# Kernel optimization log

Hardware: AMD Instinct MI355X
Metric: run time of the kernel (lower is better)

## Reference

```python
import jax, jax.numpy as jnp
import numpy as np

BUFFER_SIZE = 1024
N_BANDS = 2049
N_SPEC = 4
FRAME_SIZE = 2 * (N_BANDS - 1)  # 4096
EPS = 1e-10


def _hann_periodic(n):
    k = np.arange(n, dtype=np.float64)
    return (0.5 * (1.0 - np.cos(2.0 * np.pi * k / n))).astype(np.float32)


def _build_windows():
    # Mirrors _build_windows with nonlinearity=0 (single filterbank).
    base = _hann_periodic(FRAME_SIZE) / (FRAME_SIZE / 4.0)
    win_scale = float(base.sum())
    wins = [base.copy()]
    for lvl in range(1, N_SPEC):
        stride = 1 << lvl
        small = base[::stride][: FRAME_SIZE // stride]
        w = np.zeros(FRAME_SIZE, dtype=np.float32)
        w[-(FRAME_SIZE // stride):] = small
        w *= win_scale / w.sum()
        wins.append(w)
    return [jnp.asarray(w) for w in wins]


WINDOWS = _build_windows()


def _forward(x):
    # x: (B, BUFFER_SIZE). Fresh (reset) state: time buffers are zeros,
    # spectrogram/left-boundary buffers are +1e6 (identity for min).
    B = x.shape[0]
    T = 1 << (N_SPEC - 1)  # finest time grid = output columns
    out = jnp.full((B, N_BANDS, T), 1.0e6, dtype=x.dtype)
    pad = jnp.zeros((B, FRAME_SIZE), dtype=x.dtype)
    concat = jnp.concatenate([pad, x], axis=-1)  # (B, FRAME_SIZE + BUFFER_SIZE)
    for lvl in range(N_SPEC):
        chunk = BUFFER_SIZE >> lvl
        nfr = 1 << lvl  # sub-frames at this level
        # Overlap-save sliding windows: frame i starts at offset chunk + i*chunk
        frames = jnp.stack(
            [concat[:, chunk + i * chunk: chunk + i * chunk + FRAME_SIZE] for i in range(nfr)],
            axis=1,
        )  # (B, nfr, FRAME_SIZE)
        spec = jnp.fft.rfft(frames * WINDOWS[lvl][None, None, :], n=FRAME_SIZE, axis=-1)
        power = jnp.transpose(spec.real ** 2 + spec.imag ** 2, (0, 2, 1))  # (B, N_BANDS, nfr)
        # Upsample coarse-time levels to the finest grid (tile replication, the
        # streaming moving-max/min buffers realize this in the original) and
        # take the min across scales (buffers initialised to 1e6 = +inf for min).
        out = jnp.minimum(out, jnp.repeat(power, T // nfr, axis=-1))
    return 10.0 * jnp.log10(jnp.maximum(out, EPS))  # power -> dB


def setup_inputs() -> dict:
    key = jax.random.key(0)
    x = jax.random.normal(key, (1024, BUFFER_SIZE), dtype=jnp.float32)
    return {"x": x}


def reference(x):
    return _forward(x)
```

## Files before the change

### kernel.cpp

```cpp
#include <hip/hip_runtime.h>
#include <math.h>

#define NBANDS 2049
#define NF 4096
#define NC 2048
#define BUF 1024
#define THREADS 512
#define R2C 0.70710678118654752f

__device__ __forceinline__ int SW(int i) { return i ^ (i >> 2) ^ (i >> 6); }

__device__ __forceinline__ int posrev10(int j) {
  return ((j & 3) << 9) | (((j >> 2) & 3) << 7) | (((j >> 4) & 3) << 5) |
         (((j >> 6) & 3) << 3) | (((j >> 8) & 3) << 1);
}

struct Smem {
  float xs[BUF];
  float zreA[NC], zimA[NC];
  float zreB[NC], zimB[NC];
  float ob[4 * NBANDS];
};

struct State {
  float2 W[5];
  float2 Ub;
  float2 U1;
  float so;
  float s1a[5], s1b[5];
  float s2a[5], s2b[5];
};

__device__ __forceinline__ float2 cmul(float2 a, float2 b) {
  return make_float2(a.x * b.x - a.y * b.y, a.x * b.y + a.y * b.x);
}

template <int L>
__device__ __forceinline__ float cheb(float c) {
  #pragma unroll
  for (int i = 0; i < L; ++i) c = 2.0f * c * c - 1.0f;
  return c;
}

template <int L>
__device__ __forceinline__ void fused_s1(float* __restrict__ re, float* __restrict__ im,
                                         const Smem& sm, const State& st, int off) {
  const int n = threadIdx.x;
  constexpr int M = NF >> L;
  constexpr float ws = (float)(1 << L) * (0.5f / 1024.0f);
  const int lo = 512 - (min(off, M) >> 1);
  float dr = 0.0f, di = 0.0f;
  if (n >= lo) {
    const int idx = 2 * n + off - 1024;
    const float2 xv = *(const float2*)&sm.xs[idx];
    const float cE = cheb<L>(-st.W[0].y);
    const float cO = cheb<L>(st.so);
    dr = ws * (1.0f - cE) * xv.x;
    di = ws * (1.0f - cO) * xv.y;
  }
  const float2 W = st.W[0];
  const float2 W2 = make_float2(W.x * W.x - W.y * W.y, 2.0f * W.x * W.y);
  const float2 W3 = cmul(W, W2);
  const int p0 = SW(n), p1 = SW(n + 512), p2 = SW(n + 1024), p3 = SW(n + 1536);
  re[p0] = dr;                       im[p0] = di;
  re[p1] = -di * W.x - dr * W.y;     im[p1] = -di * W.y + dr * W.x;
  re[p2] = -(dr * W2.x - di * W2.y); im[p2] = -(dr * W2.y + di * W2.x);
  re[p3] =  di * W3.x + dr * W3.y;   im[p3] =  di * W3.y - dr * W3.x;
}

__device__ __forceinline__ void bfly4(float* __restrict__ re, float* __restrict__ im,
                                      int i0, int i1, int i2, int i3,
                                      float2 W, float2 W2, float2 W3) {
  float ar = re[i0], ai = im[i0];
  float br = re[i1], bi = im[i1];
  float cr = re[i2], ci = im[i2];
  float dr = re[i3], di = im[i3];
  float t0r = ar + cr, t0i = ai + ci;
  float t1r = ar - cr, t1i = ai - ci;
  float t2r = br + dr, t2i = bi + di;
  float t3r = br - dr, t3i = bi - di;
  re[i0] = t0r + t2r; im[i0] = t0i + t2i;
  float y1r = t1r + t3i, y1i = t1i - t3r;
  re[i1] = y1r * W.x - y1i * W.y;  im[i1] = y1r * W.y + y1i * W.x;
  float y2r = t0r - t2r, y2i = t0i - t2i;
  re[i2] = y2r * W2.x - y2i * W2.y; im[i2] = y2r * W2.y + y2i * W2.x;
  float y3r = t1r - t3i, y3i = t1i + t3r;
  re[i3] = y3r * W3.x - y3i * W3.y; im[i3] = y3r * W3.y + y3i * W3.x;
}

template <int LM, bool HASB>
__device__ __forceinline__ void radix4p(Smem& sm, float2 W) {
  const int j = threadIdx.x;
  const int m = 1 << LM;
  const int base = ((j >> LM) << (LM + 2)) | (j & (m - 1));
  const int i0 = SW(base), i1 = SW(base + m), i2 = SW(base + 2 * m), i3 = SW(base + 3 * m);
  float2 W2 = make_float2(W.x * W.x - W.y * W.y, 2.0f * W.x * W.y);
  float2 W3 = cmul(W, W2);
  bfly4(sm.zreA, sm.zimA, i0, i1, i2, i3, W, W2, W3);
  if constexpr (HASB) bfly4(sm.zreB, sm.zimB, i0, i1, i2, i3, W, W2, W3);
}

__device__ __forceinline__ void pair_powers(const float* __restrict__ re,
                                            const float* __restrict__ im,
                                            int kp, float2 U, float& pp, float& pm) {
  const int k1 = kp & (NC - 1);
  const int k2 = (NC - kp) & (NC - 1);
  const int q1 = SW(posrev10(k1 & 1023));
  const int q2 = SW(posrev10(k2 & 1023));
  const float s1 = (k1 & 1024) ? -1.0f : 1.0f;
  const float s2 = (k2 & 1024) ? -1.0f : 1.0f;
  const float zkr = re[q1] + s1 * re[q1 ^ 1];
  const float zki = im[q1] + s1 * im[q1 ^ 1];
  const float zmr = re[q2] + s2 * re[q2 ^ 1];
  const float zmi = im[q2] + s2 * im[q2 ^ 1];
  const float Ex = 0.5f * (zkr + zmr), Ey = 0.5f * (zki - zmi);
  const float Ox = 0.5f * (zki + zmi), Oy = -0.5f * (zkr - zmr);
  const float Vx = U.x * Ox - U.y * Oy, Vy = U.x * Oy + U.y * Ox;
  const float ax = Ex + Vx, ay = Ey + Vy;
  const float bx = Ex - Vx, by = Ey - Vy;
  pp = ax * ax + ay * ay;
  pm = bx * bx + by * by;
}

template <int ACT, int COL, int SLOT>
__device__ __forceinline__ void act(State& st, Smem& sm, int bin, float p) {
  if constexpr (ACT == 0)      st.s1a[SLOT] = fminf(p, 1.0e6f);
  else if constexpr (ACT == 1) st.s1b[SLOT] = fminf(p, 1.0e6f);
  else if constexpr (ACT == 2) { st.s1a[SLOT] = fminf(st.s1a[SLOT], p); st.s1b[SLOT] = fminf(st.s1b[SLOT], p); }
  else if constexpr (ACT == 3) st.s2a[SLOT] = fminf(st.s1a[SLOT], p);
  else if constexpr (ACT == 4) st.s2b[SLOT] = fminf(st.s1a[SLOT], p);
  else if constexpr (ACT == 5) st.s2a[SLOT] = fminf(st.s1b[SLOT], p);
  else if constexpr (ACT == 6) st.s2b[SLOT] = fminf(st.s1b[SLOT], p);
  else if constexpr (ACT == 7) sm.ob[COL * NBANDS + bin] = 10.0f * log10f(fmaxf(fminf(st.s2a[SLOT], p), 1.0e-10f));
  else                         sm.ob[COL * NBANDS + bin] = 10.0f * log10f(fmaxf(fminf(st.s2b[SLOT], p), 1.0e-10f));
}

template <int ACT, int COL>
__device__ __forceinline__ void unpack_frame(const float* __restrict__ re,
                                             const float* __restrict__ im,
                                             State& st, Smem& sm) {
  const int t = threadIdx.x;
  float pp, pm;
  pair_powers(re, im, t, st.Ub, pp, pm);
  act<ACT, COL, 0>(st, sm, t, pp);
  act<ACT, COL, 1>(st, sm, 2048 - t, pm);
  pair_powers(re, im, 512 + t, st.U1, pp, pm);
  act<ACT, COL, 2>(st, sm, 512 + t, pp);
  act<ACT, COL, 3>(st, sm, 1536 - t, pm);
  if (t == 0) {
    const float zr = re[0] - re[1];
    const float zi = im[0] - im[1];
    act<ACT, COL, 4>(st, sm, 1024, zr * zr + zi * zi);
  }
}

template <int LA, int ACTA, int COLA, int LB, int ACTB, int COLB, bool HASB>
__device__ __forceinline__ void pass(Smem& sm, State& st, int offA, int offB) {
  __syncthreads();
  fused_s1<LA>(sm.zreA, sm.zimA, sm, st, offA);
  if constexpr (HASB) fused_s1<LB>(sm.zreB, sm.zimB, sm, st, offB);
  __syncthreads(); radix4p<7, HASB>(sm, st.W[1]);
  __syncthreads(); radix4p<5, HASB>(sm, st.W[2]);
  __syncthreads(); radix4p<3, HASB>(sm, st.W[3]);
  __syncthreads(); radix4p<1, HASB>(sm, st.W[4]);
  __syncthreads();
  unpack_frame<ACTA, COLA>(sm.zreA, sm.zimA, st, sm);
  if constexpr (HASB) unpack_frame<ACTB, COLB>(sm.zreB, sm.zimB, st, sm);
}

template <int T0>
__device__ __forceinline__ void store_cols(Smem& sm, float* __restrict__ outb) {
  __syncthreads();
  const int tid = threadIdx.x;
  #pragma unroll
  for (int it = 0; it < 5; ++it) {
    if (it < 4 || tid == 0) {
      const int band = tid + it * THREADS;
      float4 v = make_float4(sm.ob[band], sm.ob[NBANDS + band],
                             sm.ob[2 * NBANDS + band], sm.ob[3 * NBANDS + band]);
      *(float4*)&outb[(size_t)band * 8 + T0] = v;
    }
  }
}

__global__ __launch_bounds__(THREADS, 2) void spec_kernel(const float* __restrict__ x,
                                                          float* __restrict__ out) {
  __shared__ Smem sm;
  State st;
  const int tid = threadIdx.x;
  const int b = blockIdx.x;
  const float* xb = x + (size_t)b * BUF;
  #pragma unroll
  for (int i = tid; i < BUF; i += THREADS) sm.xs[i] = xb[i];
  {
    float sn, cs;
    sincospif((float)tid * (1.0f / 1024.0f), &sn, &cs);         st.W[0] = make_float2(cs, -sn);
    sincospif((float)(tid & 127) * (1.0f / 256.0f), &sn, &cs);  st.W[1] = make_float2(cs, -sn);
    sincospif((float)(tid & 31) * (1.0f / 64.0f), &sn, &cs);    st.W[2] = make_float2(cs, -sn);
    sincospif((float)(tid & 7) * (1.0f / 16.0f), &sn, &cs);     st.W[3] = make_float2(cs, -sn);
    st.W[4] = (tid & 1) ? make_float2(R2C, -R2C) : make_float2(1.0f, 0.0f);
    sincospif((float)tid * (1.0f / 2048.0f), &sn, &cs);         st.Ub = make_float2(cs, -sn);
    st.U1 = cmul(st.Ub, make_float2(R2C, -R2C));
    sincospif((float)(2 * tid + 1) * (1.0f / 2048.0f), &sn, &cs); st.so = sn;
  }
  float* outb = out + (size_t)b * (NBANDS * 8);

  pass<1, 0, 0,  1, 1, 0, true >(sm, st, 512, 1024);
  pass<0, 2, 0,  2, 3, 0, true >(sm, st, 1024, 256);
  pass<2, 4, 0,  3, 7, 0, true >(sm, st, 512, 128);
  pass<3, 7, 1,  3, 8, 2, true >(sm, st, 256, 384);
  pass<3, 8, 3,  2, 5, 0, true >(sm, st, 512, 768);
  store_cols<0>(sm, outb);
  pass<2, 6, 0,  3, 7, 0, true >(sm, st, 1024, 640);
  pass<3, 7, 1,  3, 8, 2, true >(sm, st, 768, 896);
  pass<3, 8, 3,  0, 0, 0, false>(sm, st, 1024, 0);
  store_cols<4>(sm, outb);
}

extern "C" void kernel_launch(void* const* d_in, const int* in_sizes, int n_in,
                              void* d_out, int out_size, void* d_ws, size_t ws_size,
                              hipStream_t stream) {
  const float* x = (const float*)d_in[0];
  float* out = (float*)d_out;
  const int B = in_sizes[0] / BUF;
  hipLaunchKernelGGL(spec_kernel, dim3(B), dim3(THREADS), 0, stream, x, out);
}
```

Baseline: 102.2 us.

## Store FFT work buffers as interleaved float2 with a new bank swizzle

Changes the shared-memory FFT buffers from separate real and imaginary arrays to interleaved float2 arrays. The XOR swizzle is reworked so that 8-byte accesses avoid LDS bank conflicts, and it keeps bit 0 fixed so adjacent pairs stay contiguous. Because of that, the unpack stage can read each adjacent pair with a single 16-byte load. This halves the number of LDS instructions per butterfly and per unpack, at the risk of new bank-conflict patterns from the changed swizzle.

Measured after the change: 111.6 us. 1.09x slower.

```diff
diff --git a/kernel.cpp b/kernel.cpp
--- a/kernel.cpp
+++ b/kernel.cpp
@@ -8,7 +8,12 @@
 #define THREADS 512
 #define R2C 0.70710678118654752f
 
-__device__ __forceinline__ int SW(int i) { return i ^ (i >> 2) ^ (i >> 6); }
+__device__ __forceinline__ int SW2(int i) {
+  const int h = ((((i >> 6) ^ (i >> 7)) & 1) << 1) |
+                ((((i >> 5) ^ (i >> 8)) & 1) << 2) |
+                ((((i >> 5) ^ (i >> 9)) & 1) << 3);
+  return i ^ h;
+}
 
 __device__ __forceinline__ int posrev10(int j) {
   return ((j & 3) << 9) | (((j >> 2) & 3) << 7) | (((j >> 4) & 3) << 5) |
@@ -17,8 +22,8 @@
 
 struct Smem {
   float xs[BUF];
-  float zreA[NC], zimA[NC];
-  float zreB[NC], zimB[NC];
+  alignas(16) float2 zA[NC];
+  alignas(16) float2 zB[NC];
   float ob[4 * NBANDS];
 };
 
@@ -43,7 +48,7 @@
 }
 
 template <int L>
-__device__ __forceinline__ void fused_s1(float* __restrict__ re, float* __restrict__ im,
+__device__ __forceinline__ void fused_s1(float2* __restrict__ z,
                                          const Smem& sm, const State& st, int off) {
   const int n = threadIdx.x;
   constexpr int M = NF >> L;
@@ -61,31 +66,27 @@
   const float2 W = st.W[0];
   const float2 W2 = make_float2(W.x * W.x - W.y * W.y, 2.0f * W.x * W.y);
   const float2 W3 = cmul(W, W2);
-  const int p0 = SW(n), p1 = SW(n + 512), p2 = SW(n + 1024), p3 = SW(n + 1536);
-  re[p0] = dr;                       im[p0] = di;
-  re[p1] = -di * W.x - dr * W.y;     im[p1] = -di * W.y + dr * W.x;
-  re[p2] = -(dr * W2.x - di * W2.y); im[p2] = -(dr * W2.y + di * W2.x);
-  re[p3] =  di * W3.x + dr * W3.y;   im[p3] =  di * W3.y - dr * W3.x;
-}
-
-__device__ __forceinline__ void bfly4(float* __restrict__ re, float* __restrict__ im,
+  z[SW2(n)]        = make_float2(dr, di);
+  z[SW2(n + 512)]  = make_float2(-di * W.x - dr * W.y, -di * W.y + dr * W.x);
+  z[SW2(n + 1024)] = make_float2(-(dr * W2.x - di * W2.y), -(dr * W2.y + di * W2.x));
+  z[SW2(n + 1536)] = make_float2(di * W3.x + dr * W3.y, di * W3.y - dr * W3.x);
+}
+
+__device__ __forceinline__ void bfly4(float2* __restrict__ z,
                                       int i0, int i1, int i2, int i3,
                                       float2 W, float2 W2, float2 W3) {
-  float ar = re[i0], ai = im[i0];
-  float br = re[i1], bi = im[i1];
-  float cr = re[i2], ci = im[i2];
-  float dr = re[i3], di = im[i3];
-  float t0r = ar + cr, t0i = ai + ci;
-  float t1r = ar - cr, t1i = ai - ci;
-  float t2r = br + dr, t2i = bi + di;
-  float t3r = br - dr, t3i = bi - di;
-  re[i0] = t0r + t2r; im[i0] = t0i + t2i;
-  float y1r = t1r + t3i, y1i = t1i - t3r;
-  re[i1] = y1r * W.x - y1i * W.y;  im[i1] = y1r * W.y + y1i * W.x;
-  float y2r = t0r - t2r, y2i = t0i - t2i;
-  re[i2] = y2r * W2.x - y2i * W2.y; im[i2] = y2r * W2.y + y2i * W2.x;
-  float y3r = t1r - t3i, y3i = t1i + t3r;
-  re[i3] = y3r * W3.x - y3i * W3.y; im[i3] = y3r * W3.y + y3i * W3.x;
+  const float2 a = z[i0], b = z[i1], c = z[i2], d = z[i3];
+  const float t0r = a.x + c.x, t0i = a.y + c.y;
+  const float t1r = a.x - c.x, t1i = a.y - c.y;
+  const float t2r = b.x + d.x, t2i = b.y + d.y;
+  const float t3r = b.x - d.x, t3i = b.y - d.y;
+  z[i0] = make_float2(t0r + t2r, t0i + t2i);
+  const float y1r = t1r + t3i, y1i = t1i - t3r;
+  z[i1] = make_float2(y1r * W.x - y1i * W.y, y1r * W.y + y1i * W.x);
+  const float y2r = t0r - t2r, y2i = t0i - t2i;
+  z[i2] = make_float2(y2r * W2.x - y2i * W2.y, y2r * W2.y + y2i * W2.x);
+  const float y3r = t1r - t3i, y3i = t1i + t3r;
+  z[i3] = make_float2(y3r * W3.x - y3i * W3.y, y3r * W3.y + y3i * W3.x);
 }
 
 template <int LM, bool HASB>
@@ -93,26 +94,27 @@
   const int j = threadIdx.x;
   const int m = 1 << LM;
   const int base = ((j >> LM) << (LM + 2)) | (j & (m - 1));
-  const int i0 = SW(base), i1 = SW(base + m), i2 = SW(base + 2 * m), i3 = SW(base + 3 * m);
-  float2 W2 = make_float2(W.x * W.x - W.y * W.y, 2.0f * W.x * W.y);
-  float2 W3 = cmul(W, W2);
-  bfly4(sm.zreA, sm.zimA, i0, i1, i2, i3, W, W2, W3);
-  if constexpr (HASB) bfly4(sm.zreB, sm.zimB, i0, i1, i2, i3, W, W2, W3);
-}
-
-__device__ __forceinline__ void pair_powers(const float* __restrict__ re,
-                                            const float* __restrict__ im,
+  const int i0 = SW2(base), i1 = SW2(base + m), i2 = SW2(base + 2 * m), i3 = SW2(base + 3 * m);
+  const float2 W2 = make_float2(W.x * W.x - W.y * W.y, 2.0f * W.x * W.y);
+  const float2 W3 = cmul(W, W2);
+  bfly4(sm.zA, i0, i1, i2, i3, W, W2, W3);
+  if constexpr (HASB) bfly4(sm.zB, i0, i1, i2, i3, W, W2, W3);
+}
+
+__device__ __forceinline__ void pair_powers(const float2* __restrict__ z,
                                             int kp, float2 U, float& pp, float& pm) {
   const int k1 = kp & (NC - 1);
   const int k2 = (NC - kp) & (NC - 1);
-  const int q1 = SW(posrev10(k1 & 1023));
-  const int q2 = SW(posrev10(k2 & 1023));
+  const int q1 = SW2(posrev10(k1 & 1023));
+  const int q2 = SW2(posrev10(k2 & 1023));
   const float s1 = (k1 & 1024) ? -1.0f : 1.0f;
   const float s2 = (k2 & 1024) ? -1.0f : 1.0f;
-  const float zkr = re[q1] + s1 * re[q1 ^ 1];
-  const float zki = im[q1] + s1 * im[q1 ^ 1];
-  const float zmr = re[q2] + s2 * re[q2 ^ 1];
-  const float zmi = im[q2] + s2 * im[q2 ^ 1];
+  const float4 v1 = *(const float4*)&z[q1];
+  const float4 v2 = *(const float4*)&z[q2];
+  const float zkr = v1.x + s1 * v1.z;
+  const float zki = v1.y + s1 * v1.w;
+  const float zmr = v2.x + s2 * v2.z;
+  const float zmi = v2.y + s2 * v2.w;
   const float Ex = 0.5f * (zkr + zmr), Ey = 0.5f * (zki - zmi);
   const float Ox = 0.5f * (zki + zmi), Oy = -0.5f * (zkr - zmr);
   const float Vx = U.x * Ox - U.y * Oy, Vy = U.x * Oy + U.y * Ox;
@@ -136,20 +138,20 @@
 }
 
 template <int ACT, int COL>
-__device__ __forceinline__ void unpack_frame(const float* __restrict__ re,
-                                             const float* __restrict__ im,
+__device__ __forceinline__ void unpack_frame(const float2* __restrict__ z,
                                              State& st, Smem& sm) {
   const int t = threadIdx.x;
   float pp, pm;
-  pair_powers(re, im, t, st.Ub, pp, pm);
+  pair_powers(z, t, st.Ub, pp, pm);
   act<ACT, COL, 0>(st, sm, t, pp);
   act<ACT, COL, 1>(st, sm, 2048 - t, pm);
-  pair_powers(re, im, 512 + t, st.U1, pp, pm);
+  pair_powers(z, 512 + t, st.U1, pp, pm);
   act<ACT, COL, 2>(st, sm, 512 + t, pp);
   act<ACT, COL, 3>(st, sm, 1536 - t, pm);
   if (t == 0) {
-    const float zr = re[0] - re[1];
-    const float zi = im[0] - im[1];
+    const float4 v = *(const float4*)&z[0];
+    const float zr = v.x - v.z;
+    const float zi = v.y - v.w;
     act<ACT, COL, 4>(st, sm, 1024, zr * zr + zi * zi);
   }
 }
@@ -157,15 +159,15 @@
 template <int LA, int ACTA, int COLA, int LB, int ACTB, int COLB, bool HASB>
 __device__ __forceinline__ void pass(Smem& sm, State& st, int offA, int offB) {
   __syncthreads();
-  fused_s1<LA>(sm.zreA, sm.zimA, sm, st, offA);
-  if constexpr (HASB) fused_s1<LB>(sm.zreB, sm.zimB, sm, st, offB);
+  fused_s1<LA>(sm.zA, sm, st, offA);
+  if constexpr (HASB) fused_s1<LB>(sm.zB, sm, st, offB);
   __syncthreads(); radix4p<7, HASB>(sm, st.W[1]);
   __syncthreads(); radix4p<5, HASB>(sm, st.W[2]);
   __syncthreads(); radix4p<3, HASB>(sm, st.W[3]);
   __syncthreads(); radix4p<1, HASB>(sm, st.W[4]);
   __syncthreads();
-  unpack_frame<ACTA, COLA>(sm.zreA, sm.zimA, st, sm);
-  if constexpr (HASB) unpack_frame<ACTB, COLB>(sm.zreB, sm.zimB, st, sm);
+  unpack_frame<ACTA, COLA>(sm.zA, st, sm);
+  if constexpr (HASB) unpack_frame<ACTB, COLB>(sm.zB, st, sm);
 }
 
 template <int T0>
```
